# Performance work log

Measured on AMD Instinct MI355X. Metric: run time of the kernel, lower is better.

The kernel has to match this reference:

```python
import jax, jax.numpy as jnp
import numpy as np

NUM_ATOMS = 1024
NUM_FEATS = 80      # c
NUM_IRREPS = 48     # (l_max+1)^2 * 3 with l_max=3
K3, K2, K1 = 1270, 24, 3  # CG-basis param counts per correlation order


def setup_inputs() -> dict:
    key = jax.random.key(0)
    ks = jax.random.split(key, 7)
    return {
        "node_feats": jax.random.normal(ks[0], (NUM_ATOMS, NUM_FEATS, NUM_IRREPS), jnp.float32),
        "U3": jax.random.normal(ks[1], (NUM_IRREPS, NUM_IRREPS, NUM_IRREPS, K3), jnp.float32),
        "U2": jax.random.normal(ks[2], (NUM_IRREPS, NUM_IRREPS, K2), jnp.float32),
        "U1": jax.random.normal(ks[3], (NUM_IRREPS, K1), jnp.float32),
        "W3": jax.random.normal(ks[4], (K3, NUM_FEATS), jnp.float32),
        "W2": jax.random.normal(ks[5], (K2, NUM_FEATS), jnp.float32),
        "W1": jax.random.normal(ks[6], (K1, NUM_FEATS), jnp.float32),
    }


def reference(node_feats, U3, U2, U1, W3, W2, W1):
    # equation_main: '...ik,kc,bci -> bc...' with U3 [p,q,i,k]
    # -> out [n, c, p, q]
    out = jnp.einsum('pqik,kc,nci->ncpq', U3, W3, node_feats)

    # corr = 2: c_tensor = einsum('...k,kc->c...', U2, W2) -> [c, p, q]
    c2 = jnp.einsum('pqk,kc->cpq', U2, W2) + out          # [n, c, p, q]
    # equation_contract: 'bc...i,bci->bc...'
    out = jnp.einsum('ncpi,nci->ncp', c2, node_feats)     # [n, c, p]

    # corr = 1: c_tensor = einsum('...k,kc->c...', U1, W1) -> [c, p]
    c1 = jnp.einsum('pk,kc->cp', U1, W1) + out            # [n, c, p]
    out = jnp.einsum('nci,nci->nc', c1, node_feats)       # [n, c]
    return out
```

## Files before the change

kernel.cpp:

```cpp
#include <hip/hip_runtime.h>
#include <hip/hip_bf16.h>

#define NA 1024
#define NC 80
#define NI 48
#define PQ (NI*NI)
#define M3 (PQ*NI)
#define K3 1270
#define K3P 1280
#define K2 24
#define K1 3

typedef __attribute__((ext_vector_type(8))) short bf16x8;
typedef __attribute__((ext_vector_type(4))) float f32x4;
typedef __attribute__((ext_vector_type(4))) unsigned int u32x4;

union BFPack { bf16x8 v; __hip_bfloat162 h[4]; };
union BF4 { uint2 u; __hip_bfloat162 h[2]; };

__device__ __forceinline__ bf16x8 pack8(float a, float b, float c, float d,
                                        float e, float f, float g, float h) {
    BFPack u;
    u.h[0] = __float22bfloat162_rn(float2{a, b});
    u.h[1] = __float22bfloat162_rn(float2{c, d});
    u.h[2] = __float22bfloat162_rn(float2{e, f});
    u.h[3] = __float22bfloat162_rn(float2{g, h});
    return u.v;
}

__global__ __launch_bounds__(256) void k_w3t(const float* __restrict__ W3,
                                             __hip_bfloat16* __restrict__ W3bt) {
    int c = blockIdx.x;
    for (int k = threadIdx.x; k < K3P; k += 256) {
        float v = (k < K3) ? W3[(size_t)k * NC + c] : 0.f;
        W3bt[(size_t)c * K3P + k] = __float2bfloat16(v);
    }
}

__global__ __launch_bounds__(256) void k_uw3(const float* __restrict__ U3,
                                             const __hip_bfloat16* __restrict__ W3bt,
                                             __hip_bfloat16* __restrict__ UW3tb) {
    const int t    = threadIdx.x;
    const int wave = t >> 6;
    const int lane = t & 63;
    const int row  = lane & 15;
    const int quad = lane >> 4;

    const int m_base = blockIdx.x * 64 + wave * 16;
    const float* __restrict__ arow = U3 + (size_t)(m_base + row) * K3;

    f32x4 acc[5];
#pragma unroll
    for (int j = 0; j < 5; ++j) acc[j] = (f32x4)(0.f);

    const int kq = quad * 8;

    for (int k0 = 0; k0 < K3 - 31; k0 += 32) {
        const int kb = k0 + kq;
        const float2* a2 = (const float2*)(arow + kb);
        float2 p0 = a2[0], p1 = a2[1], p2 = a2[2], p3 = a2[3];
        bf16x8 af = pack8(p0.x, p0.y, p1.x, p1.y, p2.x, p2.y, p3.x, p3.y);
#pragma unroll
        for (int j = 0; j < 5; ++j) {
            bf16x8 bf = *(const bf16x8*)(W3bt + (size_t)(16 * j + row) * K3P + kb);
            acc[j] = __builtin_amdgcn_mfma_f32_16x16x32_bf16(af, bf, acc[j], 0, 0, 0);
        }
    }
    {
        const int kb = 1248 + kq;
        float av[8];
#pragma unroll
        for (int j = 0; j < 8; ++j) {
            int k = kb + j;
            av[j] = (k < K3) ? arow[k] : 0.f;
        }
        bf16x8 af = pack8(av[0], av[1], av[2], av[3], av[4], av[5], av[6], av[7]);
#pragma unroll
        for (int j = 0; j < 5; ++j) {
            bf16x8 bf = *(const bf16x8*)(W3bt + (size_t)(16 * j + row) * K3P + kb);
            acc[j] = __builtin_amdgcn_mfma_f32_16x16x32_bf16(af, bf, acc[j], 0, 0, 0);
        }
    }

#pragma unroll
    for (int j = 0; j < 5; ++j) {
        int c = 16 * j + row;
        size_t o = (size_t)c * M3 + m_base + quad * 4;
        BF4 pk;
        pk.h[0] = __float22bfloat162_rn(float2{acc[j].x, acc[j].y});
        pk.h[1] = __float22bfloat162_rn(float2{acc[j].z, acc[j].w});
        *(uint2*)&UW3tb[o] = pk.u;
    }
}

__global__ __launch_bounds__(256) void k_c2t(const float* __restrict__ U2,
                                             const float* __restrict__ W2,
                                             float* __restrict__ c2t) {
    int idx = blockIdx.x * 256 + threadIdx.x;
    if (idx >= NC * PQ) return;
    int c  = idx / PQ;
    int pq = idx - c * PQ;
    float s = 0.f;
#pragma unroll
    for (int k = 0; k < K2; ++k) s += U2[pq * K2 + k] * W2[k * NC + c];
    c2t[idx] = s;
}

__global__ __launch_bounds__(256) void k_main(const float* __restrict__ nf,
                                              const __hip_bfloat16* __restrict__ UW3tb,
                                              const float* __restrict__ c2t,
                                              const float* __restrict__ U1,
                                              const float* __restrict__ W1,
                                              float* __restrict__ out) {
    __shared__ __align__(16) float Vs[64 * 52];
    __shared__ __align__(16) union { unsigned short vb[64 * 64];
                                     float red[64 * 17]; } VbRed;
    __shared__ __align__(16) unsigned short Ts[64 * 64];
    __shared__ __align__(16) float c2s[64];
    __shared__ __align__(16) float c1s[NI];

    const int t    = threadIdx.x;
    const int wave = t >> 6;
    const int col  = t & 15;
    const int quad = (t >> 4) & 3;

    const int bid = blockIdx.x;
    const int xcd = bid & 7;
    const int kb_ = bid >> 3;
    const int c   = xcd + 8 * (kb_ >> 4);
    const int nb  = kb_ & 15;
    const int n0  = nb * 64;

#pragma unroll
    for (int u = 0; u < 3; ++u) {
        int f   = t + 256 * u;
        int row = f / 12;
        int seg = f - row * 12;
        float4 v = *(const float4*)&nf[((size_t)(n0 + row) * NC + c) * NI + seg * 4];
        *(float4*)&Vs[row * 52 + seg * 4] = v;
        BF4 pk;
        pk.h[0] = __float22bfloat162_rn(float2{v.x, v.y});
        pk.h[1] = __float22bfloat162_rn(float2{v.z, v.w});
        *(uint2*)((char*)VbRed.vb + row * 128 + ((seg * 8) ^ ((row & 7) << 4))) = pk.u;
    }
    if (t < 128) {
        int row = t >> 1;
        int off = ((6 + (t & 1)) * 16) ^ ((row & 7) << 4);
        u32x4 z = (u32x4)(0u);
        *(u32x4*)((char*)VbRed.vb + row * 128 + off) = z;
        *(u32x4*)((char*)Ts       + row * 128 + off) = z;
    }
    if (t < NI) {
        float s = 0.f;
#pragma unroll
        for (int k = 0; k < K1; ++k) s += U1[t * K1 + k] * W1[k * NC + c];
        c1s[t] = s;
    }

    const __hip_bfloat16* Tcb = UW3tb + (size_t)c * M3;
    u32x4 pre0, pre1;
    pre0 = *(const u32x4*)(Tcb + (size_t)t * 8);
    if (t < 128) pre1 = *(const u32x4*)(Tcb + (size_t)(t + 256) * 8);

    __syncthreads();

    bf16x8 bfr[2][4];
#pragma unroll
    for (int s = 0; s < 2; ++s)
#pragma unroll
        for (int g = 0; g < 4; ++g) {
            int rw = 16 * g + col;
            bfr[s][g] = *(const bf16x8*)((const char*)VbRed.vb + rw * 128 +
                                         ((s * 64 + quad * 16) ^ ((rw & 7) << 4)));
        }
    int n52[4];
#pragma unroll
    for (int g = 0; g < 4; ++g) n52[g] = (16 * g + col) * 52;

    const int arow  = 16 * wave + col;
    const int abase = arow * 128;
    const int aswz  = (arow & 7) << 4;
    const int wq16  = 16 * wave + quad * 4;

    float oacc[4] = {0.f, 0.f, 0.f, 0.f};

    for (int tile = 0; tile < PQ / 64; ++tile) {
        __syncthreads();
        {
            int row = t / 6, seg = t - row * 6;
            *(u32x4*)((char*)Ts + row * 128 + ((seg * 16) ^ ((row & 7) << 4))) = pre0;
            if (t < 128) {
                int f2 = t + 256;
                int row2 = f2 / 6, seg2 = f2 - row2 * 6;
                *(u32x4*)((char*)Ts + row2 * 128 + ((seg2 * 16) ^ ((row2 & 7) << 4))) = pre1;
            }
        }
        if (t < 64) c2s[t] = c2t[(size_t)c * PQ + tile * 64 + t];
        __syncthreads();

        {
            int nt = (tile + 1 < PQ / 64) ? tile + 1 : tile;
            const __hip_bfloat16* src = Tcb + (size_t)nt * (64 * NI);
            pre0 = *(const u32x4*)(src + (size_t)t * 8);
            if (t < 128) pre1 = *(const u32x4*)(src + (size_t)(t + 256) * 8);
        }

        f32x4 acc[4];
#pragma unroll
        for (int g = 0; g < 4; ++g) acc[g] = (f32x4)(0.f);
#pragma unroll
        for (int s = 0; s < 2; ++s) {
            bf16x8 af = *(const bf16x8*)((const char*)Ts + abase +
                                         ((s * 64 + quad * 16) ^ aswz));
#pragma unroll
            for (int g = 0; g < 4; ++g)
                acc[g] = __builtin_amdgcn_mfma_f32_16x16x32_bf16(af, bfr[s][g], acc[g], 0, 0, 0);
        }

        int pqb = tile * 64 + wq16;
        int p   = (pqb * 21846) >> 20;
        int q0  = pqb - p * 48;
        f32x4 cv = *(const f32x4*)&c2s[wq16];
#pragma unroll
        for (int g = 0; g < 4; ++g) {
            float vp = Vs[n52[g] + p];
            f32x4 vq = *(const f32x4*)&Vs[n52[g] + q0];
#pragma unroll
            for (int r = 0; r < 4; ++r)
                oacc[g] += (acc[g][r] + cv[r]) * vp * vq[r];
        }
    }

    __syncthreads();
#pragma unroll
    for (int g = 0; g < 4; ++g)
        VbRed.red[(16 * g + col) * 17 + (t >> 4)] = oacc[g];
    __syncthreads();
    if (t < 64) {
        float s = 0.f;
#pragma unroll
        for (int j = 0; j < 16; ++j) s += VbRed.red[t * 17 + j];
#pragma unroll
        for (int p = 0; p < NI; ++p) s += c1s[p] * Vs[t * 52 + p];
        out[(size_t)(n0 + t) * NC + c] = s;
    }
}

extern "C" void kernel_launch(void* const* d_in, const int* in_sizes, int n_in,
                              void* d_out, int out_size, void* d_ws, size_t ws_size,
                              hipStream_t stream) {
    const float* nf = (const float*)d_in[0];
    const float* U3 = (const float*)d_in[1];
    const float* U2 = (const float*)d_in[2];
    const float* U1 = (const float*)d_in[3];
    const float* W3 = (const float*)d_in[4];
    const float* W2 = (const float*)d_in[5];
    const float* W1 = (const float*)d_in[6];
    float* out = (float*)d_out;

    __hip_bfloat16* UW3tb = (__hip_bfloat16*)d_ws;
    float* c2tw = (float*)((char*)d_ws + (size_t)NC * M3 * 2);
    __hip_bfloat16* W3bt = (__hip_bfloat16*)c2tw;

    k_w3t <<<NC,                    256, 0, stream>>>(W3, W3bt);
    k_uw3 <<<M3 / 64,               256, 0, stream>>>(U3, W3bt, UW3tb);
    k_c2t <<<(NC * PQ + 255) / 256, 256, 0, stream>>>(U2, W2, c2tw);
    k_main<<<NC * 16,               256, 0, stream>>>(nf, UW3tb, c2tw, U1, W1, out);
}
```

Before: 943.7 us.

## Stage U3 and W3 tiles through swizzled LDS with register prefetch in k_uw3

The U3·W3 GEMM kernel now loads 64-wide K tiles of A (converted to bf16) and B into shared memory with an XOR swizzle. It reads MFMA operands from LDS instead of issuing strided global loads per lane. The next tile is prefetched into registers while the current tile is computed, which overlaps global latency with MFMA work and makes the global reads coalesced. The cost is two barriers per tile and more LDS and register use, which could lower occupancy.

New measurement: 814.9 us. -13.7%, faster.

```diff
diff --git a/kernel.cpp b/kernel.cpp
--- a/kernel.cpp
+++ b/kernel.cpp
@@ -40,52 +40,104 @@
 __global__ __launch_bounds__(256) void k_uw3(const float* __restrict__ U3,
                                              const __hip_bfloat16* __restrict__ W3bt,
                                              __hip_bfloat16* __restrict__ UW3tb) {
+    __shared__ __align__(16) unsigned short As[64 * 64];
+    __shared__ __align__(16) unsigned short Bs[80 * 64];
+
     const int t    = threadIdx.x;
     const int wave = t >> 6;
     const int lane = t & 63;
-    const int row  = lane & 15;
+    const int col  = lane & 15;
     const int quad = lane >> 4;
 
-    const int m_base = blockIdx.x * 64 + wave * 16;
-    const float* __restrict__ arow = U3 + (size_t)(m_base + row) * K3;
+    const int m_base = blockIdx.x * 64;
+
+    const int ar  = t >> 2;
+    const int cg  = t & 3;
+    const float* __restrict__ arow = U3 + (size_t)(m_base + ar) * K3 + cg * 16;
+    const int rA   = 16 * wave + col;
+    const int aswz = rA & 7;
 
     f32x4 acc[5];
 #pragma unroll
     for (int j = 0; j < 5; ++j) acc[j] = (f32x4)(0.f);
 
-    const int kq = quad * 8;
-
-    for (int k0 = 0; k0 < K3 - 31; k0 += 32) {
-        const int kb = k0 + kq;
-        const float2* a2 = (const float2*)(arow + kb);
-        float2 p0 = a2[0], p1 = a2[1], p2 = a2[2], p3 = a2[3];
-        bf16x8 af = pack8(p0.x, p0.y, p1.x, p1.y, p2.x, p2.y, p3.x, p3.y);
-#pragma unroll
-        for (int j = 0; j < 5; ++j) {
-            bf16x8 bf = *(const bf16x8*)(W3bt + (size_t)(16 * j + row) * K3P + kb);
-            acc[j] = __builtin_amdgcn_mfma_f32_16x16x32_bf16(af, bf, acc[j], 0, 0, 0);
-        }
-    }
-    {
-        const int kb = 1248 + kq;
-        float av[8];
-#pragma unroll
-        for (int j = 0; j < 8; ++j) {
-            int k = kb + j;
-            av[j] = (k < K3) ? arow[k] : 0.f;
-        }
-        bf16x8 af = pack8(av[0], av[1], av[2], av[3], av[4], av[5], av[6], av[7]);
-#pragma unroll
-        for (int j = 0; j < 5; ++j) {
-            bf16x8 bf = *(const bf16x8*)(W3bt + (size_t)(16 * j + row) * K3P + kb);
-            acc[j] = __builtin_amdgcn_mfma_f32_16x16x32_bf16(af, bf, acc[j], 0, 0, 0);
+    float2 preA[8];
+    u32x4  preB[3];
+
+#pragma unroll
+    for (int j = 0; j < 8; ++j) preA[j] = *(const float2*)(arow + j * 2);
+#pragma unroll
+    for (int u = 0; u < 3; ++u) {
+        if (u < 2 || t < 128) {
+            int g = t + 256 * u;
+            int c = g >> 3, gk = g & 7;
+            preB[u] = *(const u32x4*)(W3bt + (size_t)c * K3P + gk * 8);
+        }
+    }
+
+    for (int tile = 0; tile < 20; ++tile) {
+        __syncthreads();
+        {
+            bf16x8 g0 = pack8(preA[0].x, preA[0].y, preA[1].x, preA[1].y,
+                              preA[2].x, preA[2].y, preA[3].x, preA[3].y);
+            bf16x8 g1 = pack8(preA[4].x, preA[4].y, preA[5].x, preA[5].y,
+                              preA[6].x, preA[6].y, preA[7].x, preA[7].y);
+            *(bf16x8*)((char*)As + ar * 128 + (((cg * 2 + 0) ^ (ar & 7)) * 16)) = g0;
+            *(bf16x8*)((char*)As + ar * 128 + (((cg * 2 + 1) ^ (ar & 7)) * 16)) = g1;
+        }
+#pragma unroll
+        for (int u = 0; u < 3; ++u) {
+            if (u < 2 || t < 128) {
+                int g = t + 256 * u;
+                int c = g >> 3, gk = g & 7;
+                *(u32x4*)((char*)Bs + c * 128 + ((gk ^ (c & 7)) * 16)) = preB[u];
+            }
+        }
+        __syncthreads();
+
+        if (tile + 1 < 20) {
+            int nt = tile + 1;
+            int k0 = nt * 64;
+            if (nt == 19) {
+#pragma unroll
+                for (int j = 0; j < 8; ++j) {
+                    int k = k0 + cg * 16 + j * 2;
+                    preA[j] = (k < K3) ? *(const float2*)(arow + k0 + j * 2)
+                                       : float2{0.f, 0.f};
+                }
+            } else {
+#pragma unroll
+                for (int j = 0; j < 8; ++j)
+                    preA[j] = *(const float2*)(arow + k0 + j * 2);
+            }
+#pragma unroll
+            for (int u = 0; u < 3; ++u) {
+                if (u < 2 || t < 128) {
+                    int g = t + 256 * u;
+                    int c = g >> 3, gk = g & 7;
+                    preB[u] = *(const u32x4*)(W3bt + (size_t)c * K3P + k0 + gk * 8);
+                }
+            }
+        }
+
+#pragma unroll
+        for (int s = 0; s < 2; ++s) {
+            bf16x8 af = *(const bf16x8*)((const char*)As + rA * 128 +
+                                         (((s * 4 + quad) ^ aswz) * 16));
+#pragma unroll
+            for (int j = 0; j < 5; ++j) {
+                int cr = 16 * j + col;
+                bf16x8 bf = *(const bf16x8*)((const char*)Bs + cr * 128 +
+                                             (((s * 4 + quad) ^ (cr & 7)) * 16));
+                acc[j] = __builtin_amdgcn_mfma_f32_16x16x32_bf16(af, bf, acc[j], 0, 0, 0);
+            }
         }
     }
 
 #pragma unroll
     for (int j = 0; j < 5; ++j) {
-        int c = 16 * j + row;
-        size_t o = (size_t)c * M3 + m_base + quad * 4;
+        int c = 16 * j + col;
+        size_t o = (size_t)c * M3 + m_base + 16 * wave + quad * 4;
         BF4 pk;
         pk.h[0] = __float22bfloat162_rn(float2{acc[j].x, acc[j].y});
         pk.h[1] = __float22bfloat162_rn(float2{acc[j].z, acc[j].w});
```

## Stage U3/W3 tiles through swizzled LDS with register prefetch in UW3 GEMM

Applied to the files above, without the earlier changes.

Reworks the U3×W3 bf16 MFMA GEMM so that each block loads 128-wide K tiles of A and B cooperatively with coalesced global reads. The tiles are converted to bf16 and stored in XOR-swizzled shared memory to avoid bank conflicts. The next tile is prefetched into registers while MFMAs run on the current one. This targets the uncoalesced per-lane strided loads of U3 rows and the repeated global reads of W3. In exchange it adds two barriers per tile and extra register pressure from the prefetch buffers.

Measured after the change: 810.6 us. 1.16x faster.

```diff
diff --git a/kernel.cpp b/kernel.cpp
--- a/kernel.cpp
+++ b/kernel.cpp
@@ -17,6 +17,7 @@
 
 union BFPack { bf16x8 v; __hip_bfloat162 h[4]; };
 union BF4 { uint2 u; __hip_bfloat162 h[2]; };
+union BF2 { unsigned int u; __hip_bfloat162 h; };
 
 __device__ __forceinline__ bf16x8 pack8(float a, float b, float c, float d,
                                         float e, float f, float g, float h) {
@@ -40,52 +41,88 @@
 __global__ __launch_bounds__(256) void k_uw3(const float* __restrict__ U3,
                                              const __hip_bfloat16* __restrict__ W3bt,
                                              __hip_bfloat16* __restrict__ UW3tb) {
+    __shared__ __align__(16) unsigned short As[64 * 128];
+    __shared__ __align__(16) unsigned short Bs[80 * 128];
+
     const int t    = threadIdx.x;
     const int wave = t >> 6;
     const int lane = t & 63;
-    const int row  = lane & 15;
+    const int col  = lane & 15;
     const int quad = lane >> 4;
 
-    const int m_base = blockIdx.x * 64 + wave * 16;
-    const float* __restrict__ arow = U3 + (size_t)(m_base + row) * K3;
+    const int m_base = blockIdx.x * 64;
+
+    const float* __restrict__ aw = U3 + (size_t)(m_base + 16 * wave) * K3 + 2 * lane;
+    char* asw = (char*)As + (16 * wave) * 256 + (lane & 3) * 4;
+    const int ag = lane >> 2;
 
     f32x4 acc[5];
 #pragma unroll
     for (int j = 0; j < 5; ++j) acc[j] = (f32x4)(0.f);
 
-    const int kq = quad * 8;
-
-    for (int k0 = 0; k0 < K3 - 31; k0 += 32) {
-        const int kb = k0 + kq;
-        const float2* a2 = (const float2*)(arow + kb);
-        float2 p0 = a2[0], p1 = a2[1], p2 = a2[2], p3 = a2[3];
-        bf16x8 af = pack8(p0.x, p0.y, p1.x, p1.y, p2.x, p2.y, p3.x, p3.y);
-#pragma unroll
-        for (int j = 0; j < 5; ++j) {
-            bf16x8 bf = *(const bf16x8*)(W3bt + (size_t)(16 * j + row) * K3P + kb);
-            acc[j] = __builtin_amdgcn_mfma_f32_16x16x32_bf16(af, bf, acc[j], 0, 0, 0);
-        }
-    }
-    {
-        const int kb = 1248 + kq;
-        float av[8];
-#pragma unroll
-        for (int j = 0; j < 8; ++j) {
-            int k = kb + j;
-            av[j] = (k < K3) ? arow[k] : 0.f;
-        }
-        bf16x8 af = pack8(av[0], av[1], av[2], av[3], av[4], av[5], av[6], av[7]);
-#pragma unroll
-        for (int j = 0; j < 5; ++j) {
-            bf16x8 bf = *(const bf16x8*)(W3bt + (size_t)(16 * j + row) * K3P + kb);
-            acc[j] = __builtin_amdgcn_mfma_f32_16x16x32_bf16(af, bf, acc[j], 0, 0, 0);
+    float2 preA[16];
+    u32x4  preB[5];
+
+#pragma unroll
+    for (int s = 0; s < 16; ++s)
+        preA[s] = *(const float2*)(aw + (size_t)s * K3);
+#pragma unroll
+    for (int u = 0; u < 5; ++u) {
+        int G = t + 256 * u, c = G >> 4, g = G & 15;
+        preB[u] = *(const u32x4*)(W3bt + (size_t)c * K3P + g * 8);
+    }
+
+    for (int tile = 0; tile < 10; ++tile) {
+        __syncthreads();
+#pragma unroll
+        for (int s = 0; s < 16; ++s) {
+            BF2 w; w.h = __float22bfloat162_rn(preA[s]);
+            *(unsigned int*)(asw + s * 256 + ((ag ^ (s & 7)) * 16)) = w.u;
+        }
+#pragma unroll
+        for (int u = 0; u < 5; ++u) {
+            int G = t + 256 * u, c = G >> 4, g = G & 15;
+            *(u32x4*)((char*)Bs + c * 256 + ((g ^ (c & 7)) * 16)) = preB[u];
+        }
+        __syncthreads();
+
+        if (tile < 9) {
+            const int k0 = (tile + 1) * 128;
+            const float* an = aw + k0;
+            if (tile + 1 == 9) {
+#pragma unroll
+                for (int s = 0; s < 16; ++s)
+                    preA[s] = (lane < 59) ? *(const float2*)(an + (size_t)s * K3)
+                                          : float2{0.f, 0.f};
+            } else {
+#pragma unroll
+                for (int s = 0; s < 16; ++s)
+                    preA[s] = *(const float2*)(an + (size_t)s * K3);
+            }
+#pragma unroll
+            for (int u = 0; u < 5; ++u) {
+                int G = t + 256 * u, c = G >> 4, g = G & 15;
+                preB[u] = *(const u32x4*)(W3bt + (size_t)c * K3P + k0 + g * 8);
+            }
+        }
+
+        const int rbase = (16 * wave + col) * 256;
+#pragma unroll
+        for (int ks = 0; ks < 4; ++ks) {
+            const int go = ((ks * 4 + quad) ^ (col & 7)) * 16;
+            bf16x8 af = *(const bf16x8*)((const char*)As + rbase + go);
+#pragma unroll
+            for (int j = 0; j < 5; ++j) {
+                bf16x8 bf = *(const bf16x8*)((const char*)Bs + (16 * j + col) * 256 + go);
+                acc[j] = __builtin_amdgcn_mfma_f32_16x16x32_bf16(af, bf, acc[j], 0, 0, 0);
+            }
         }
     }
 
 #pragma unroll
     for (int j = 0; j < 5; ++j) {
-        int c = 16 * j + row;
-        size_t o = (size_t)c * M3 + m_base + quad * 4;
+        int c = 16 * j + col;
+        size_t o = (size_t)c * M3 + m_base + 16 * wave + quad * 4;
         BF4 pk;
         pk.h[0] = __float22bfloat162_rn(float2{acc[j].x, acc[j].y});
         pk.h[1] = __float22bfloat162_rn(float2{acc[j].z, acc[j].w});
```
